# Kernel optimization log

Hardware: AMD Instinct MI355X
Metric: run time of the kernel (lower is better)

The kernel has to match this reference:

```python
import jax, jax.numpy as jnp
import numpy as np

B, S, H, R, G, L, A = 1024, 512, 2048, 64, 16, 4, 256
ADAPT_SCALE = 0.1


def setup_inputs() -> dict:
    key = jax.random.key(0)
    ks = jax.random.split(key, 12)
    w = lambda k, shp: (jax.random.normal(k, shp, dtype=jnp.float32) * 0.02)
    return {
        "s": jax.random.normal(ks[0], (B, S), dtype=jnp.float32),
        "W_in": w(ks[1], (S, H)),
        "b_in": jnp.zeros((H,), jnp.float32),
        "W_main": w(ks[2], (L, H, H)),
        "b_main": jnp.zeros((L, H), jnp.float32),
        "Wa": w(ks[3], (L, G, H, R)),   # down-projection per layer/group
        "ba": jnp.zeros((L, G, R), jnp.float32),
        "Wb": w(ks[4], (L, G, R, H)),   # up-projection per layer/group
        "bb": jnp.zeros((L, G, H), jnp.float32),
        "W_out": w(ks[5], (H, A)),
        "b_out": jnp.zeros((A,), jnp.float32),
    }


def reference(s, W_in, b_in, W_main, b_main, Wa, ba, Wb, bb, W_out, b_out):
    # g=None path: expand state across groups, then input layer (group-invariant)
    x = s @ W_in + b_in                              # [B, H]
    x = jnp.broadcast_to(x[:, None, :], (B, G, H))   # [B, G, H]
    for i in range(L):
        h = jnp.einsum("bgh,hk->bgk", x, W_main[i]) + b_main[i]          # shared main GEMM
        z = jnp.einsum("bgh,ghr->bgr", x, Wa[i]) + ba[i]                  # grouped low-rank down
        z = jnp.einsum("bgr,grh->bgh", z, Wb[i]) + bb[i]                  # grouped low-rank up
        h = h + ADAPT_SCALE * z
        x = jax.nn.elu(h)                            # dropout in eval mode = identity
    logits = jnp.einsum("bgh,ha->bga", x, W_out) + b_out  # Categorical(logits=...)
    return logits
```

## Files before the change

### kernel.cpp

```cpp
#include <hip/hip_runtime.h>
#include <cstdint>
#include <cmath>

typedef _Float16 f16;
typedef _Float16 f16x8 __attribute__((ext_vector_type(8)));
typedef float f32x4 __attribute__((ext_vector_type(4)));

#define DEVI static __device__ __forceinline__

constexpr int B_ = 1024, S_ = 512, H_ = 2048, R_ = 64, G_ = 16, L_ = 4, A_ = 256;
constexpr float ADAPT = 0.1f;

DEVI void gl_lds16(const void* g, void* l) {
  __builtin_amdgcn_global_load_lds((const __attribute__((address_space(1))) void*)g,
                                   (__attribute__((address_space(3))) void*)l,
                                   16, 0, 0);
}

__global__ void cvt_f16_kernel(const float* __restrict__ src, f16* __restrict__ dst, int n) {
  int i = blockIdx.x * blockDim.x + threadIdx.x;
  if (i < n) dst[i] = (f16)src[i];
}

__global__ void transpose_cvt_kernel(const float* __restrict__ src, f16* __restrict__ dst,
                                     int rows, int cols, float scale) {
  src += (size_t)blockIdx.z * rows * cols;
  dst += (size_t)blockIdx.z * rows * cols;
  __shared__ float tile[32][33];
  const int tx = threadIdx.x, ty = threadIdx.y;
  const int r0 = blockIdx.y * 32, c0 = blockIdx.x * 32;
  #pragma unroll
  for (int i = ty; i < 32; i += 8)
    tile[i][tx] = src[(size_t)(r0 + i) * cols + (c0 + tx)];
  __syncthreads();
  #pragma unroll
  for (int i = ty; i < 32; i += 8)
    dst[(size_t)(c0 + i) * rows + (r0 + tx)] = (f16)(tile[tx][i] * scale);
}


#define MQ(QM, QN, AF, BF)                                                   \
  _Pragma("unroll") for (int i = 0; i < 4; ++i)                              \
  _Pragma("unroll") for (int j = 0; j < 2; ++j)                              \
  _Pragma("unroll") for (int k = 0; k < 2; ++k)                              \
    acc[QM][QN][i][j] = __builtin_amdgcn_mfma_f32_16x16x32_f16(              \
        AF[i][k], BF[j][k], acc[QM][QN][i][j], 0, 0, 0)

#define STGM(BASE, OFF, DST) do {                                            \
    gl_lds16(BASE + OFF, &lds[DST]);                                         \
    gl_lds16(BASE + OFF + 32768, &lds[DST + 1024]);                          \
    OFF += 128; DST ^= 65536; } while (0)
#define STGC(BASE, OFF, DST) do {                                            \
    gl_lds16(BASE + OFF, &lds[DST]);                                         \
    gl_lds16(BASE + OFF + 1024, &lds[DST + 1024]);                           \
    DST ^= 65536; } while (0)
#define NOSTG ((void)0)
#define WV6 asm volatile("s_waitcnt vmcnt(6)")
#define WV0 asm volatile("s_waitcnt vmcnt(0)")
#define NOW ((void)0)

#define TILE_BODY(S1, S2, S3, S4, BW) do {                                   \
    f16x8 a0[4][2], a1[4][2], b0[2][2], b1v[2][2];                           \
    _Pragma("unroll") for (int i = 0; i < 4; ++i) {                          \
      a0[i][0] = *(const f16x8*)&lds[cab + i * 2048 + lof0];                 \
      a0[i][1] = *(const f16x8*)&lds[cab + i * 2048 + lof1]; }               \
    _Pragma("unroll") for (int j = 0; j < 2; ++j) {                          \
      b0[j][0] = *(const f16x8*)&lds[cbb + j * 2048 + lof0];                 \
      b0[j][1] = *(const f16x8*)&lds[cbb + j * 2048 + lof1]; }               \
    S1;                                                                      \
    __builtin_amdgcn_s_barrier();                                            \
    __builtin_amdgcn_s_setprio(1);                                           \
    MQ(0, 0, a0, b0);                                                        \
    __builtin_amdgcn_s_setprio(0);                                           \
    __builtin_amdgcn_s_barrier();                                            \
    _Pragma("unroll") for (int j = 0; j < 2; ++j) {                          \
      b1v[j][0] = *(const f16x8*)&lds[cbb + 16384 + j * 2048 + lof0];        \
      b1v[j][1] = *(const f16x8*)&lds[cbb + 16384 + j * 2048 + lof1]; }      \
    S2;                                                                      \
    __builtin_amdgcn_s_barrier();                                            \
    __builtin_amdgcn_s_setprio(1);                                           \
    MQ(0, 1, a0, b1v);                                                       \
    __builtin_amdgcn_s_setprio(0);                                           \
    __builtin_amdgcn_s_barrier();                                            \
    _Pragma("unroll") for (int i = 0; i < 4; ++i) {                          \
      a1[i][0] = *(const f16x8*)&lds[cab + 16384 + i * 2048 + lof0];         \
      a1[i][1] = *(const f16x8*)&lds[cab + 16384 + i * 2048 + lof1]; }       \
    S3;                                                                      \
    __builtin_amdgcn_s_barrier();                                            \
    __builtin_amdgcn_s_setprio(1);                                           \
    MQ(1, 1, a1, b1v);                                                       \
    __builtin_amdgcn_s_setprio(0);                                           \
    __builtin_amdgcn_s_barrier();                                            \
    S4;                                                                      \
    __builtin_amdgcn_s_barrier();                                            \
    __builtin_amdgcn_s_setprio(1);                                           \
    MQ(1, 0, a1, b0);                                                        \
    __builtin_amdgcn_s_setprio(0);                                           \
    BW;                                                                      \
    __builtin_amdgcn_s_barrier();                                            \
    cab ^= 65536; cbb ^= 65536;                                              \
  } while (0)

__global__ __launch_bounds__(512, 2)
void gemm8_main_kernel(const f16* __restrict__ Aacts,
                      const f16* __restrict__ Wm,
                      const f16* __restrict__ Z1,
                      const f16* __restrict__ Wb2,
                      const float* __restrict__ b1,
                      const float* __restrict__ b2,
                      f16* __restrict__ Out) {
  __shared__ __align__(16) char lds[131072];
  const int tid = threadIdx.x, lane = tid & 63, wid = tid >> 6;
  const int swz = (blockIdx.x & 7) * 64 + (blockIdx.x >> 3);
  const int bm0 = (swz & 63) * 256, bn0 = (swz >> 6) * 256;
  const int g = bm0 >> 10;
  const char* GA = (const char*)Aacts;
  const char* GB = (const char*)Wm;
  const char* GZ = (const char*)Z1;
  const char* GW2 = (const char*)(Wb2 + (size_t)g * H_ * R_);
  const float* b2g = b2 + (size_t)g * H_;

  const int srow8 = lane >> 3;
  const int scolb = ((lane & 7) ^ srow8) * 16;
  const int fr = lane & 15, fq = lane >> 4;
  const uint32_t lof0 = fr * 128 + ((fq * 16) ^ ((fr & 7) << 4));
  const uint32_t lof1 = lof0 ^ 64;

  const uint32_t rA0 = bm0 + wid * 16 + srow8;
  const uint32_t rB0 = bn0 + wid * 16 + srow8;
  uint32_t oA0 = rA0 * 4096 + scolb;
  uint32_t oA1 = oA0 + 128 * 4096;
  uint32_t oB0 = rB0 * 4096 + scolb;
  uint32_t oB1 = oB0 + 128 * 4096;
  uint32_t dA0 = wid * 2048;
  uint32_t dA1 = 16384 + wid * 2048;
  uint32_t dB0 = 32768 + wid * 2048;
  uint32_t dB1 = 49152 + wid * 2048;
  uint32_t cab = (wid >> 2) * 8192;
  uint32_t cbb = 32768 + (wid & 3) * 4096;

  f32x4 acc[2][2][4][2] = {};

  STGM(GA, oA0, dA0);
  STGM(GB, oB0, dB0);
  STGM(GA, oA1, dA1);
  STGM(GB, oB1, dB1);
  STGM(GA, oA0, dA0);
  STGM(GB, oB0, dB0);
  STGM(GA, oA1, dA1);
  WV6;
  __builtin_amdgcn_s_barrier();

  for (int t = 0; t < 30; ++t)
    TILE_BODY(STGM(GB, oB1, dB1), STGM(GA, oA0, dA0),
              STGM(GB, oB0, dB0), STGM(GA, oA1, dA1), WV6);

  {
    uint32_t oA0c = rA0 * 128 + scolb;
    uint32_t oA1c = oA0c + 128 * 128;
    uint32_t oB0c = rB0 * 128 + scolb;
    uint32_t oB1c = oB0c + 128 * 128;
    TILE_BODY(STGM(GB, oB1, dB1), STGC(GZ, oA0c, dA0),
              STGC(GW2, oB0c, dB0), STGC(GZ, oA1c, dA1), WV6);
    TILE_BODY(STGC(GW2, oB1c, dB1), NOSTG, NOSTG, NOSTG, WV0);
  }
  TILE_BODY(NOSTG, NOSTG, NOSTG, NOSTG, NOW);

  #pragma unroll
  for (int Qn = 0; Qn < 2; ++Qn) {
    #pragma unroll
    for (int j = 0; j < 2; ++j) {
      const int col = bn0 + Qn * 128 + (wid & 3) * 32 + j * 16 + fr;
      const float bb1 = b1[col];
      const float bb2 = ADAPT * b2g[col];
      #pragma unroll
      for (int Qm = 0; Qm < 2; ++Qm) {
        #pragma unroll
        for (int i = 0; i < 4; ++i) {
          #pragma unroll
          for (int r = 0; r < 4; ++r) {
            const int row = bm0 + Qm * 128 + (wid >> 2) * 64 + i * 16 + fq * 4 + r;
            float v = acc[Qm][Qn][i][j][r] + bb1 + bb2;
            v = v > 0.f ? v : expm1f(v);
            Out[(size_t)row * H_ + col] = (f16)v;
          }
        }
      }
    }
  }
}

enum { EPI_Z1 = 0, EPI_MAIN = 1, EPI_OUT = 2, EPI_L0 = 3 };

template <int BM, int BN, int WM, int WN, int EPI>
__global__ __launch_bounds__((BM / WM) * (BN / WN) * 64)
void gemm_f16_kernel(const f16* __restrict__ A, long long lda, long long Az,
                     const f16* __restrict__ Bw, long long ldb, long long Bz,
                     const f16* __restrict__ A2, long long lda2,
                     const f16* __restrict__ B2w, long long ldb2, long long B2z,
                     int NT1, int NT2,
                     const float* __restrict__ bias1, long long b1z,
                     const float* __restrict__ bias2, long long b2z,
                     const f16* __restrict__ addmat,
                     void* __restrict__ outp, long long out_z, long long ldo,
                     int rows_per_group) {
  constexpr int NW = (BM / WM) * (BN / WN);
  constexpr int FM = WM / 16, FN = WN / 16;
  constexpr int RA = BM / (NW * 16), RB = BN / (NW * 16);
  const int tid = threadIdx.x, lane = tid & 63, wid = tid >> 6;
  const int bm0 = blockIdx.x * BM, bn0 = blockIdx.y * BN;
  const int z = blockIdx.z;
  const int gidx = (rows_per_group > 0) ? (bm0 / rows_per_group) : 0;

  __shared__ __align__(16) f16 As[BM * 32];
  __shared__ __align__(16) f16 Bs[BN * 32];

  const int wm0 = (wid / (BN / WN)) * WM;
  const int wn0 = (wid % (BN / WN)) * WN;
  const int srow = wid * 16 + (lane >> 2);
  const int scol = (lane & 3) * 8;
  const int fr = lane & 15, fq = lane >> 4;

  f32x4 acc[FM][FN] = {};

  const f16* arp = &As[(wm0 + fr) * 32 + fq * 8];
  const f16* brp = &Bs[(wn0 + fr) * 32 + fq * 8];
  auto compute = [&]() {
    f16x8 af[FM], bf[FN];
    #pragma unroll
    for (int i = 0; i < FM; ++i) af[i] = *(const f16x8*)(arp + i * 16 * 32);
    #pragma unroll
    for (int j = 0; j < FN; ++j) bf[j] = *(const f16x8*)(brp + j * 16 * 32);
    #pragma unroll
    for (int i = 0; i < FM; ++i)
      #pragma unroll
      for (int j = 0; j < FN; ++j)
        acc[i][j] = __builtin_amdgcn_mfma_f32_16x16x32_f16(af[i], bf[j], acc[i][j], 0, 0, 0);
  };

  if (NT1 > 0) {
    const f16* pa = A + (long long)z * Az + (long long)(bm0 + srow) * lda + scol;
    const f16* pb = Bw + (long long)z * Bz + (long long)(bn0 + srow) * ldb + scol;
    const long long stA = (long long)(NW * 16) * lda;
    const long long stB = (long long)(NW * 16) * ldb;
    for (int kt = 0; kt < NT1; ++kt) {
      #pragma unroll
      for (int r = 0; r < RA; ++r) gl_lds16(pa + r * stA, &As[(r * NW + wid) * 512]);
      #pragma unroll
      for (int r = 0; r < RB; ++r) gl_lds16(pb + r * stB, &Bs[(r * NW + wid) * 512]);
      pa += 32; pb += 32;
      __syncthreads();
      compute();
      __syncthreads();
    }
  }
  if (NT2 > 0) {
    const f16* pa = A2 + (long long)(bm0 + srow) * lda2 + scol;
    const f16* pb = B2w + (long long)gidx * B2z + (long long)(bn0 + srow) * ldb2 + scol;
    const long long stA = (long long)(NW * 16) * lda2;
    const long long stB = (long long)(NW * 16) * ldb2;
    for (int kt = 0; kt < NT2; ++kt) {
      #pragma unroll
      for (int r = 0; r < RA; ++r) gl_lds16(pa + r * stA, &As[(r * NW + wid) * 512]);
      #pragma unroll
      for (int r = 0; r < RB; ++r) gl_lds16(pb + r * stB, &Bs[(r * NW + wid) * 512]);
      pa += 32; pb += 32;
      __syncthreads();
      compute();
      __syncthreads();
    }
  }

  const float* b1p = bias1 ? bias1 + (long long)z * b1z : nullptr;
  const float* b2p = bias2 ? bias2 + (long long)gidx * b2z : nullptr;
  #pragma unroll
  for (int i = 0; i < FM; ++i) {
    #pragma unroll
    for (int j = 0; j < FN; ++j) {
      const int col = bn0 + wn0 + j * 16 + fr;
      const float b1 = b1p ? b1p[col] : 0.f;
      const float b2v = b2p ? ADAPT * b2p[col] : 0.f;
      #pragma unroll
      for (int r = 0; r < 4; ++r) {
        const int row = bm0 + wm0 + i * 16 + fq * 4 + r;
        float v = acc[i][j][r] + b1 + b2v;
        if constexpr (EPI == EPI_MAIN) {
          v = v > 0.f ? v : expm1f(v);
          ((f16*)outp)[(long long)row * ldo + col] = (f16)v;
        } else if constexpr (EPI == EPI_L0) {
          v += (float)addmat[(long long)(row & (B_ - 1)) * H_ + col];
          v = v > 0.f ? v : expm1f(v);
          ((f16*)outp)[(long long)row * ldo + col] = (f16)v;
        } else if constexpr (EPI == EPI_Z1) {
          ((f16*)outp)[(long long)z * out_z + (long long)row * ldo + col] = (f16)v;
        } else {
          const int g = row >> 10, b = row & 1023;
          ((float*)outp)[((long long)b * G_ + g) * A_ + col] = v;
        }
      }
    }
  }
}

extern "C" void kernel_launch(void* const* d_in, const int* in_sizes, int n_in,
                              void* d_out, int out_size, void* d_ws, size_t ws_size,
                              hipStream_t stream) {
  const float* s      = (const float*)d_in[0];
  const float* W_in   = (const float*)d_in[1];
  const float* b_in   = (const float*)d_in[2];
  const float* W_main = (const float*)d_in[3];
  const float* b_main = (const float*)d_in[4];
  const float* Wa     = (const float*)d_in[5];
  const float* ba     = (const float*)d_in[6];
  const float* Wb     = (const float*)d_in[7];
  const float* bb     = (const float*)d_in[8];
  const float* W_out  = (const float*)d_in[9];
  const float* b_out  = (const float*)d_in[10];

  char* ws = (char*)d_ws;
  size_t off = 0;
  auto alloc = [&](size_t bytes) -> void* {
    void* p = ws + off;
    off += (bytes + 255) & ~(size_t)255;
    return p;
  };
  f16* sh   = (f16*)alloc((size_t)B_ * S_ * 2);
  f16* Wint = (f16*)alloc((size_t)H_ * S_ * 2);
  f16* Wmt  = (f16*)alloc((size_t)L_ * H_ * H_ * 2);
  f16* Wat  = (f16*)alloc((size_t)L_ * G_ * R_ * H_ * 2);
  f16* Wbt  = (f16*)alloc((size_t)L_ * G_ * H_ * R_ * 2);
  f16* Wot  = (f16*)alloc((size_t)A_ * H_ * 2);
  f16* xh0  = (f16*)alloc((size_t)G_ * B_ * H_ * 2);
  f16* xh1  = (f16*)alloc((size_t)G_ * B_ * H_ * 2);
  f16* z1h  = (f16*)alloc((size_t)G_ * B_ * R_ * 2);
  f16* x0h  = xh1;
  f16* y0h  = xh1 + (size_t)B_ * H_;

  cvt_f16_kernel<<<(B_ * S_ + 255) / 256, 256, 0, stream>>>(s, sh, B_ * S_);
  dim3 tb(32, 8);
  transpose_cvt_kernel<<<dim3(H_ / 32, S_ / 32, 1),   tb, 0, stream>>>(W_in,   Wint, S_, H_, 1.f);
  transpose_cvt_kernel<<<dim3(H_ / 32, H_ / 32, L_),  tb, 0, stream>>>(W_main, Wmt,  H_, H_, 1.f);
  transpose_cvt_kernel<<<dim3(R_ / 32, H_ / 32, L_ * G_), tb, 0, stream>>>(Wa, Wat, H_, R_, 1.f);
  transpose_cvt_kernel<<<dim3(H_ / 32, R_ / 32, L_ * G_), tb, 0, stream>>>(Wb, Wbt, R_, H_, ADAPT);
  transpose_cvt_kernel<<<dim3(A_ / 32, H_ / 32, 1),   tb, 0, stream>>>(W_out,  Wot,  H_, A_, 1.f);

  gemm_f16_kernel<64, 128, 32, 64, EPI_Z1><<<dim3(B_ / 64, H_ / 128, 1), 256, 0, stream>>>(
      sh, S_, 0, Wint, S_, 0, nullptr, 0, nullptr, 0, 0,
      S_ / 32, 0, b_in, 0, nullptr, 0, nullptr, x0h, 0, H_, 0);

  gemm_f16_kernel<64, 128, 32, 64, EPI_Z1><<<dim3(B_ / 64, H_ / 128, 1), 256, 0, stream>>>(
      x0h, H_, 0, Wmt, H_, 0, nullptr, 0, nullptr, 0, 0,
      H_ / 32, 0, b_main, 0, nullptr, 0, nullptr, y0h, 0, H_, 0);

  gemm_f16_kernel<64, 64, 32, 32, EPI_Z1><<<dim3(B_ / 64, 1, G_), 256, 0, stream>>>(
      x0h, H_, 0, Wat, H_, (long long)R_ * H_, nullptr, 0, nullptr, 0, 0,
      H_ / 32, 0, ba, R_, nullptr, 0, nullptr, z1h, (long long)B_ * R_, R_, 0);

  gemm_f16_kernel<128, 128, 64, 64, EPI_L0><<<dim3(G_ * B_ / 128, H_ / 128, 1), 256, 0, stream>>>(
      nullptr, 0, 0, nullptr, 0, 0, z1h, R_, Wbt, R_, (long long)H_ * R_,
      0, R_ / 32, nullptr, 0, bb, H_, y0h, xh0, 0, H_, B_);

  f16* cur = xh0;
  f16* nxt = xh1;
  for (int l = 1; l < L_; ++l) {
    gemm_f16_kernel<64, 64, 32, 32, EPI_Z1><<<dim3(B_ / 64, 1, G_), 256, 0, stream>>>(
        cur, H_, (long long)B_ * H_,
        Wat + (size_t)l * G_ * R_ * H_, H_, (long long)R_ * H_,
        nullptr, 0, nullptr, 0, 0,
        H_ / 32, 0,
        ba + (size_t)l * G_ * R_, R_, nullptr, 0, nullptr,
        z1h, (long long)B_ * R_, R_, 0);
    gemm8_main_kernel<<<512, 512, 0, stream>>>(
        cur, Wmt + (size_t)l * H_ * H_, z1h, Wbt + (size_t)l * G_ * H_ * R_,
        b_main + (size_t)l * H_, bb + (size_t)l * G_ * H_, nxt);
    f16* t = cur; cur = nxt; nxt = t;
  }

  gemm_f16_kernel<128, 128, 64, 64, EPI_OUT><<<dim3(G_ * B_ / 128, A_ / 128, 1), 256, 0, stream>>>(
      cur, H_, 0, Wot, H_, 0, nullptr, 0, nullptr, 0, 0,
      H_ / 32, 0, b_out, 0, nullptr, 0, nullptr, d_out, 0, A_, 0);
}
```

Baseline: 798.4 us.

## Prefetch next tile's LDS fragments and use finer vmcnt waits in main GEMM

Restructures the main GEMM K-loop so the A0/B0 fragments for the next tile are read from LDS at the end of the current tile, overlapping those reads with the last MFMA quadrant. It also tightens per-phase s_waitcnt vmcnt values, unrolls by two with fixed buffer offsets instead of toggling cab/cbb, and adds sched_barrier after each s_barrier to pin instruction order. This aims to hide LDS read latency and reduce stalls, at the cost of more live fragment registers, which may hurt occupancy at 2 blocks of 512 threads.

After: 1.259 ms. 57.7% more time.

```diff
diff --git a/kernel.cpp b/kernel.cpp
--- a/kernel.cpp
+++ b/kernel.cpp
@@ -55,50 +55,39 @@
     gl_lds16(BASE + OFF + 1024, &lds[DST + 1024]);                           \
     DST ^= 65536; } while (0)
 #define NOSTG ((void)0)
+#define WV8 asm volatile("s_waitcnt vmcnt(8)")
 #define WV6 asm volatile("s_waitcnt vmcnt(6)")
+#define WV4 asm volatile("s_waitcnt vmcnt(4)")
 #define WV0 asm volatile("s_waitcnt vmcnt(0)")
 #define NOW ((void)0)
-
-#define TILE_BODY(S1, S2, S3, S4, BW) do {                                   \
-    f16x8 a0[4][2], a1[4][2], b0[2][2], b1v[2][2];                           \
-    _Pragma("unroll") for (int i = 0; i < 4; ++i) {                          \
-      a0[i][0] = *(const f16x8*)&lds[cab + i * 2048 + lof0];                 \
-      a0[i][1] = *(const f16x8*)&lds[cab + i * 2048 + lof1]; }               \
-    _Pragma("unroll") for (int j = 0; j < 2; ++j) {                          \
-      b0[j][0] = *(const f16x8*)&lds[cbb + j * 2048 + lof0];                 \
-      b0[j][1] = *(const f16x8*)&lds[cbb + j * 2048 + lof1]; }               \
-    S1;                                                                      \
-    __builtin_amdgcn_s_barrier();                                            \
-    __builtin_amdgcn_s_setprio(1);                                           \
-    MQ(0, 0, a0, b0);                                                        \
-    __builtin_amdgcn_s_setprio(0);                                           \
-    __builtin_amdgcn_s_barrier();                                            \
-    _Pragma("unroll") for (int j = 0; j < 2; ++j) {                          \
-      b1v[j][0] = *(const f16x8*)&lds[cbb + 16384 + j * 2048 + lof0];        \
-      b1v[j][1] = *(const f16x8*)&lds[cbb + 16384 + j * 2048 + lof1]; }      \
-    S2;                                                                      \
-    __builtin_amdgcn_s_barrier();                                            \
-    __builtin_amdgcn_s_setprio(1);                                           \
-    MQ(0, 1, a0, b1v);                                                       \
-    __builtin_amdgcn_s_setprio(0);                                           \
-    __builtin_amdgcn_s_barrier();                                            \
-    _Pragma("unroll") for (int i = 0; i < 4; ++i) {                          \
-      a1[i][0] = *(const f16x8*)&lds[cab + 16384 + i * 2048 + lof0];         \
-      a1[i][1] = *(const f16x8*)&lds[cab + 16384 + i * 2048 + lof1]; }       \
-    S3;                                                                      \
-    __builtin_amdgcn_s_barrier();                                            \
-    __builtin_amdgcn_s_setprio(1);                                           \
-    MQ(1, 1, a1, b1v);                                                       \
-    __builtin_amdgcn_s_setprio(0);                                           \
-    __builtin_amdgcn_s_barrier();                                            \
-    S4;                                                                      \
-    __builtin_amdgcn_s_barrier();                                            \
-    __builtin_amdgcn_s_setprio(1);                                           \
-    MQ(1, 0, a1, b0);                                                        \
-    __builtin_amdgcn_s_setprio(0);                                           \
-    BW;                                                                      \
-    __builtin_amdgcn_s_barrier();                                            \
-    cab ^= 65536; cbb ^= 65536;                                              \
+#define NORD ((void)0)
+#define BARS do { __builtin_amdgcn_s_barrier(); \
+                  __builtin_amdgcn_sched_barrier(0); } while (0)
+#define PRI1 __builtin_amdgcn_s_setprio(1)
+#define PRI0 __builtin_amdgcn_s_setprio(0)
+
+#define RD_A0(P) do { _Pragma("unroll") for (int i = 0; i < 4; ++i) {        \
+    fa0[i][0] = *(const f16x8*)&lds[(P) + cab + i * 2048 + lof0];            \
+    fa0[i][1] = *(const f16x8*)&lds[(P) + cab + i * 2048 + lof1]; } } while (0)
+#define RD_A1(P) do { _Pragma("unroll") for (int i = 0; i < 4; ++i) {        \
+    fa1[i][0] = *(const f16x8*)&lds[(P) + cab + 16384 + i * 2048 + lof0];    \
+    fa1[i][1] = *(const f16x8*)&lds[(P) + cab + 16384 + i * 2048 + lof1]; } } while (0)
+#define RD_B0(P) do { _Pragma("unroll") for (int j = 0; j < 2; ++j) {        \
+    fb0[j][0] = *(const f16x8*)&lds[(P) + cbb + j * 2048 + lof0];            \
+    fb0[j][1] = *(const f16x8*)&lds[(P) + cbb + j * 2048 + lof1]; } } while (0)
+#define RD_B1(P) do { _Pragma("unroll") for (int j = 0; j < 2; ++j) {        \
+    fb1[j][0] = *(const f16x8*)&lds[(P) + cbb + 16384 + j * 2048 + lof0];    \
+    fb1[j][1] = *(const f16x8*)&lds[(P) + cbb + 16384 + j * 2048 + lof1]; } } while (0)
+
+#define TILE(PC, PN, S1, S2, S3, S4, W2, W3, W4, RD3, RD4) do {              \
+    RD_B1(PC); S1; BARS;                                                     \
+    PRI1; MQ(0, 0, fa0, fb0); PRI0; BARS;                                    \
+    RD_A1(PC); S2; W2; BARS;                                                 \
+    PRI1; MQ(0, 1, fa0, fb1); PRI0; BARS;                                    \
+    RD3; S3; W3; BARS;                                                       \
+    PRI1; MQ(1, 1, fa1, fb1); PRI0; BARS;                                    \
+    S4; BARS;                                                                \
+    PRI1; MQ(1, 0, fa1, fb0); PRI0; RD4; W4; BARS;                           \
   } while (0)
 
 __global__ __launch_bounds__(512, 2)
@@ -136,10 +125,11 @@
   uint32_t dA1 = 16384 + wid * 2048;
   uint32_t dB0 = 32768 + wid * 2048;
   uint32_t dB1 = 49152 + wid * 2048;
-  uint32_t cab = (wid >> 2) * 8192;
-  uint32_t cbb = 32768 + (wid & 3) * 4096;
+  const uint32_t cab = (wid >> 2) * 8192;
+  const uint32_t cbb = 32768 + (wid & 3) * 4096;
 
   f32x4 acc[2][2][4][2] = {};
+  f16x8 fa0[4][2], fa1[4][2], fb0[2][2], fb1[2][2];
 
   STGM(GA, oA0, dA0);
   STGM(GB, oB0, dB0);
@@ -149,22 +139,36 @@
   STGM(GB, oB0, dB0);
   STGM(GA, oA1, dA1);
   WV6;
-  __builtin_amdgcn_s_barrier();
-
-  for (int t = 0; t < 30; ++t)
-    TILE_BODY(STGM(GB, oB1, dB1), STGM(GA, oA0, dA0),
-              STGM(GB, oB0, dB0), STGM(GA, oA1, dA1), WV6);
+  BARS;
+  RD_A0(0);
+  RD_B0(0);
+
+  #pragma unroll 1
+  for (int it = 0; it < 15; ++it) {
+    TILE(0, 65536,
+         STGM(GB, oB1, dB1), STGM(GA, oA0, dA0),
+         STGM(GB, oB0, dB0), STGM(GA, oA1, dA1),
+         WV8, WV8, WV6, RD_A0(65536), RD_B0(65536));
+    TILE(65536, 0,
+         STGM(GB, oB1, dB1), STGM(GA, oA0, dA0),
+         STGM(GB, oB0, dB0), STGM(GA, oA1, dA1),
+         WV8, WV8, WV6, RD_A0(0), RD_B0(0));
+  }
 
   {
     uint32_t oA0c = rA0 * 128 + scolb;
     uint32_t oA1c = oA0c + 128 * 128;
     uint32_t oB0c = rB0 * 128 + scolb;
     uint32_t oB1c = oB0c + 128 * 128;
-    TILE_BODY(STGM(GB, oB1, dB1), STGC(GZ, oA0c, dA0),
-              STGC(GW2, oB0c, dB0), STGC(GZ, oA1c, dA1), WV6);
-    TILE_BODY(STGC(GW2, oB1c, dB1), NOSTG, NOSTG, NOSTG, WV0);
-  }
-  TILE_BODY(NOSTG, NOSTG, NOSTG, NOSTG, NOW);
+    TILE(0, 65536,
+         STGM(GB, oB1, dB1), STGC(GZ, oA0c, dA0),
+         STGC(GW2, oB0c, dB0), STGC(GZ, oA1c, dA1),
+         WV8, WV8, WV6, RD_A0(65536), RD_B0(65536));
+    TILE(65536, 0,
+         STGC(GW2, oB1c, dB1), NOSTG, NOSTG, NOSTG,
+         WV6, WV4, WV0, RD_A0(0), RD_B0(0));
+  }
+  TILE(0, 65536, NOSTG, NOSTG, NOSTG, NOSTG, NOW, NOW, NOW, NORD, NORD);
 
   #pragma unroll
   for (int Qn = 0; Qn < 2; ++Qn) {
```
